# Kernel optimization log

Measured on AMD Instinct MI355X. Metric: run time of the kernel, lower is better.

## Reference

```python
import jax, jax.numpy as jnp
import numpy as np

NGRAM = 16
SUB = 512  # bytes per sub-block


def byte2image(block, ngram=NGRAM):
    """block: (B, L) int -> (B, 1, ngram*8, L-ngram) float32 in [-1, 1]."""
    B, L = block.shape
    blk = block.astype(jnp.int32)
    # nxt[:, i] = blk[:, i+1], last column zero
    nxt = jnp.concatenate([blk[:, 1:], jnp.zeros((B, 1), jnp.int32)], axis=1)
    # 8 bit-shifted views of the byte stream
    shifts = jnp.stack(
        [((blk << s) & 255) + ((nxt >> (8 - s)) & 255) for s in range(8)],
        axis=1,
    )  # (B, 8, L)
    flat = shifts.reshape(B, -1)  # (B, 8*L)
    parts = [flat] + [jnp.roll(flat, -i, axis=1) for i in range(1, ngram)]
    stacked = jnp.concatenate(parts, axis=1).reshape(B, ngram * 8, L)
    result = stacked[:, :, :-ngram].astype(jnp.float32)
    result = (result / 255.0 - 0.5) / 0.5
    return result[:, None]  # (B, 1, ngram*8, L-ngram)


def byte2image_4k(block, ngram=NGRAM):
    """block: (B, 4096) -> (B, 8, ngram*8, 512-ngram)."""
    return jnp.concatenate(
        [byte2image(block[:, i * SUB:(i + 1) * SUB], ngram) for i in range(8)],
        axis=1,
    )


def setup_inputs() -> dict:
    key = jax.random.key(0)
    kx, kw = jax.random.split(key)
    x = jax.random.randint(kx, (256, 4096), 0, 256, dtype=jnp.int64)
    W = jax.random.normal(kw, (496, 64), dtype=jnp.float32) * 0.02
    return {"x": x, "W": W}


def reference(x, W):
    # ByteFormerWrapper.forward with block_size=4096: byte2image_4k then the
    # (opaque) model; model stood in by a linear head over the image width.
    img = byte2image_4k(x)                      # (B, 8, 128, 496)
    out = jnp.einsum('bchw,wo->bcho', img, W)   # (B, 8, 128, 64)
    return out
```

## Files before the change

kernel.cpp:

```cpp
#include <hip/hip_runtime.h>

typedef unsigned short u16;
typedef unsigned int u32;
typedef _Float16 half8 __attribute__((ext_vector_type(8)));
typedef __attribute__((ext_vector_type(4))) float floatx4;

#define LSTRIDE 72
#define BIMG (128 * LSTRIDE)

__device__ __forceinline__ void gl_lds16(const void* g, void* l) {
  __builtin_amdgcn_global_load_lds(
      (const __attribute__((address_space(1))) void*)g,
      (__attribute__((address_space(3))) void*)l, 16, 0, 0);
}
__device__ __forceinline__ void gl_lds4(const void* g, void* l) {
  __builtin_amdgcn_global_load_lds(
      (const __attribute__((address_space(1))) void*)g,
      (__attribute__((address_space(3))) void*)l, 4, 0, 0);
}

__global__ __launch_bounds__(256) void byteformer_precompute(
    const float* __restrict__ Wm, u16* __restrict__ Bws,
    float* __restrict__ csumWs) {
  const int t = threadIdx.x;
  const int y = blockIdx.x >> 3, kc = blockIdx.x & 7;
  const int wave = t >> 6, o = t & 63;
  const int pp = wave >> 1, hf = wave & 1;
  u16* img = Bws + (size_t)blockIdx.x * BIMG;
  #pragma unroll
  for (int i = 0; i < 18; ++i) {
    const int kk = (hf * 18 + i) * 2;
    u32 val = 0u;
    if (kk < 64) {
      const int c0 = kc * 64 + kk - 2 * y - pp;
      const int c1 = c0 + 1;
      float f0 = (c0 >= 0 && c0 < 496) ? Wm[c0 * 64 + o] : 0.0f;
      float f1 = (c1 >= 0 && c1 < 496) ? Wm[c1 * 64 + o] : 0.0f;
      u16 h0 = __builtin_bit_cast(unsigned short, (_Float16)f0);
      u16 h1 = __builtin_bit_cast(unsigned short, (_Float16)f1);
      val = (u32)h0 | ((u32)h1 << 16);
    }
    *(u32*)&img[(pp * 64 + o) * LSTRIDE + kk] = val;
  }
  if (blockIdx.x == 0) {
    __shared__ float red[256];
    float s = 0.0f;
    for (int c = wave * 124; c < wave * 124 + 124; ++c) s += Wm[c * 64 + o];
    red[t] = s;
    __syncthreads();
    if (t < 64)
      csumWs[t] = (1024.0f * (2.0f / 255.0f) + 1.0f) *
                  (red[t] + red[t + 64] + red[t + 128] + red[t + 192]);
  }
}

__global__ __launch_bounds__(256, 4) void byteformer_fused(
    const int* __restrict__ x, const u16* __restrict__ Bws,
    const float* __restrict__ csumWs, float* __restrict__ out) {
  __shared__ __align__(16) u16 As[128 * LSTRIDE];
  __shared__ __align__(16) u16 Bs[128 * LSTRIDE];

  const int t = threadIdx.x;
  const int mtile = blockIdx.x;
  const int n0 = blockIdx.y * 128;

  const int wave = t >> 6, lane = t & 63;
  const int wm = wave >> 1, wn = wave & 1;
  const int quad = lane >> 4, l16 = lane & 15;

  const int sA_sub = t >> 4;
  const int sA_kg  = (t >> 1) & 7;
  const int sA_qh  = t & 1;
  const long xrow = ((long)mtile * 16 + sA_sub) * 512;

  const char* bimg0 = (const char*)(Bws + (size_t)blockIdx.y * 8 * BIMG);

  floatx4 acc[4][4];
  #pragma unroll
  for (int mt = 0; mt < 4; ++mt)
    #pragma unroll
    for (int nt = 0; nt < 4; ++nt)
      acc[mt][nt] = floatx4{0.f, 0.f, 0.f, 0.f};

  int4 ca, cb; int cc;
  {
    const int base = sA_kg * 8;
    ca = *(const int4*)&x[xrow + base];
    cb = *(const int4*)&x[xrow + base + 4];
    cc = x[xrow + base + 8];
  }

  for (int kc = 0; kc < 8; ++kc) {
    __syncthreads();

    {
      const char* src = bimg0 + (size_t)kc * (BIMG * 2);
      char* dst = (char*)Bs;
      const int woff = wave * 1024;
      #pragma unroll
      for (int j = 0; j < 4; ++j)
        gl_lds16(src + j * 4096 + woff + lane * 16, dst + j * 4096 + woff);
      const int woff4 = 16384 + wave * 256;
      #pragma unroll
      for (int j = 0; j < 2; ++j)
        gl_lds4(src + woff4 + j * 1024 + lane * 4, dst + woff4 + j * 1024);
    }

    {
      const u32 c0 = (u32)ca.x, c1 = (u32)ca.y, c2 = (u32)ca.z, c3 = (u32)ca.w;
      const u32 c4 = (u32)cb.x, c5 = (u32)cb.y, c6 = (u32)cb.z, c7 = (u32)cb.w;
      const u32 c8 = (u32)cc;
      const u32 P0 = ((c0 << 8) | c1) | (((c1 << 8) | c2) << 16);
      const u32 P1 = ((c2 << 8) | c3) | (((c3 << 8) | c4) << 16);
      const u32 P2 = ((c4 << 8) | c5) | (((c5 << 8) | c6) << 16);
      const u32 P3 = ((c6 << 8) | c7) | (((c7 << 8) | c8) << 16);
      u16* arow = &As[(sA_sub * 8 + sA_qh * 4) * LSTRIDE + sA_kg * 8];
      #pragma unroll
      for (int qi = 0; qi < 4; ++qi) {
        const int sh = 8 - (sA_qh * 4 + qi);
        int4 d;
        d.x = (int)(((P0 >> sh) & 0x00FF00FFu) | 0x64006400u);
        d.y = (int)(((P1 >> sh) & 0x00FF00FFu) | 0x64006400u);
        d.z = (int)(((P2 >> sh) & 0x00FF00FFu) | 0x64006400u);
        d.w = (int)(((P3 >> sh) & 0x00FF00FFu) | 0x64006400u);
        *(int4*)(arow + qi * LSTRIDE) = d;
      }
    }

    __syncthreads();

    if (kc < 7) {
      const int base = (kc + 1) * 64 + sA_kg * 8;
      ca = *(const int4*)&x[xrow + base];
      cb = *(const int4*)&x[xrow + base + 4];
      cc = (base + 8 < 512) ? x[xrow + base + 8] : 0;
    }

    #pragma unroll
    for (int ks = 0; ks < 2; ++ks) {
      const int koff = ks * 32 + quad * 8;
      half8 af[4], bf[4];
      #pragma unroll
      for (int mt = 0; mt < 4; ++mt)
        af[mt] = *(const half8*)&As[(wm * 64 + mt * 16 + l16) * LSTRIDE + koff];
      #pragma unroll
      for (int nt = 0; nt < 4; ++nt)
        bf[nt] = *(const half8*)&Bs[(wn * 64 + nt * 16 + l16) * LSTRIDE + koff];
      #pragma unroll
      for (int mt = 0; mt < 4; ++mt)
        #pragma unroll
        for (int nt = 0; nt < 4; ++nt)
          acc[mt][nt] = __builtin_amdgcn_mfma_f32_16x16x32_f16(
              af[mt], bf[nt], acc[mt][nt], 0, 0, 0);
    }
  }

  const float S = 2.0f / 255.0f;
  #pragma unroll
  for (int nt = 0; nt < 4; ++nt) {
    int n = n0 + wn * 64 + nt * 16 + l16;
    int p = n >> 6, o = n & 63;
    float cs = csumWs[o];
    #pragma unroll
    for (int mt = 0; mt < 4; ++mt) {
      int mbase = mtile * 128 + wm * 64 + mt * 16 + quad * 4;
      #pragma unroll
      for (int i = 0; i < 4; ++i) {
        int mr = mbase + i;
        int sub = mr >> 3, q = mr & 7;
        out[(long)sub * 8192 + (p * 8 + q) * 64 + o] = S * acc[mt][nt][i] - cs;
      }
    }
  }
}

extern "C" void kernel_launch(void* const* d_in, const int* in_sizes, int n_in,
                              void* d_out, int out_size, void* d_ws, size_t ws_size,
                              hipStream_t stream) {
  const int* x = (const int*)d_in[0];
  const float* Wm = (const float*)d_in[1];
  float* out = (float*)d_out;
  u16* Bws = (u16*)d_ws;
  float* csumWs = (float*)((char*)d_ws + (size_t)64 * BIMG * 2);
  byteformer_precompute<<<dim3(64), dim3(256), 0, stream>>>(Wm, Bws, csumWs);
  byteformer_fused<<<dim3(128, 8), dim3(256), 0, stream>>>(x, Bws, csumWs, out);
}
```

Baseline: 117.6 us.

## Double-buffer A/B LDS tiles and stage epilogue through LDS for coalesced stores

Allocates two LDS buffers each for the A and B tiles so that the next chunk's x load, B DMA and A bit-unpacking overlap with the current MFMA compute, cutting one barrier per iteration. The epilogue writes results into LDS and then issues coalesced float4 global stores instead of scattered scalar stores, with the csum values hoisted into registers. Launch bounds drop to 2 blocks per CU because LDS use doubles, which reduces occupancy in exchange for overlap.

```diff
diff --git a/kernel.cpp b/kernel.cpp
--- a/kernel.cpp
+++ b/kernel.cpp
@@ -54,15 +54,14 @@
   }
 }
 
-__global__ __launch_bounds__(256, 4) void byteformer_fused(
+__global__ __launch_bounds__(256, 2) void byteformer_fused(
     const int* __restrict__ x, const u16* __restrict__ Bws,
     const float* __restrict__ csumWs, float* __restrict__ out) {
-  __shared__ __align__(16) u16 As[128 * LSTRIDE];
-  __shared__ __align__(16) u16 Bs[128 * LSTRIDE];
+  __shared__ __align__(16) u16 arena[4 * BIMG];
 
   const int t = threadIdx.x;
   const int mtile = blockIdx.x;
-  const int n0 = blockIdx.y * 128;
+  const int y = blockIdx.y;
 
   const int wave = t >> 6, lane = t & 63;
   const int wm = wave >> 1, wn = wave & 1;
@@ -72,8 +71,7 @@
   const int sA_kg  = (t >> 1) & 7;
   const int sA_qh  = t & 1;
   const long xrow = ((long)mtile * 16 + sA_sub) * 512;
-
-  const char* bimg0 = (const char*)(Bws + (size_t)blockIdx.y * 8 * BIMG);
+  const char* bimg0 = (const char*)(Bws + (size_t)y * 8 * BIMG);
 
   floatx4 acc[4][4];
   #pragma unroll
@@ -82,70 +80,63 @@
     for (int nt = 0; nt < 4; ++nt)
       acc[mt][nt] = floatx4{0.f, 0.f, 0.f, 0.f};
 
+  float cs[4];
+  #pragma unroll
+  for (int nt = 0; nt < 4; ++nt) cs[nt] = csumWs[nt * 16 + l16];
+
   int4 ca, cb; int cc;
-  {
-    const int base = sA_kg * 8;
+  auto xload = [&](int kc) {
+    const int base = kc * 64 + sA_kg * 8;
     ca = *(const int4*)&x[xrow + base];
     cb = *(const int4*)&x[xrow + base + 4];
-    cc = x[xrow + base + 8];
-  }
-
-  for (int kc = 0; kc < 8; ++kc) {
-    __syncthreads();
-
-    {
-      const char* src = bimg0 + (size_t)kc * (BIMG * 2);
-      char* dst = (char*)Bs;
-      const int woff = wave * 1024;
-      #pragma unroll
-      for (int j = 0; j < 4; ++j)
-        gl_lds16(src + j * 4096 + woff + lane * 16, dst + j * 4096 + woff);
-      const int woff4 = 16384 + wave * 256;
-      #pragma unroll
-      for (int j = 0; j < 2; ++j)
-        gl_lds4(src + woff4 + j * 1024 + lane * 4, dst + woff4 + j * 1024);
-    }
-
-    {
-      const u32 c0 = (u32)ca.x, c1 = (u32)ca.y, c2 = (u32)ca.z, c3 = (u32)ca.w;
-      const u32 c4 = (u32)cb.x, c5 = (u32)cb.y, c6 = (u32)cb.z, c7 = (u32)cb.w;
-      const u32 c8 = (u32)cc;
-      const u32 P0 = ((c0 << 8) | c1) | (((c1 << 8) | c2) << 16);
-      const u32 P1 = ((c2 << 8) | c3) | (((c3 << 8) | c4) << 16);
-      const u32 P2 = ((c4 << 8) | c5) | (((c5 << 8) | c6) << 16);
-      const u32 P3 = ((c6 << 8) | c7) | (((c7 << 8) | c8) << 16);
-      u16* arow = &As[(sA_sub * 8 + sA_qh * 4) * LSTRIDE + sA_kg * 8];
-      #pragma unroll
-      for (int qi = 0; qi < 4; ++qi) {
-        const int sh = 8 - (sA_qh * 4 + qi);
-        int4 d;
-        d.x = (int)(((P0 >> sh) & 0x00FF00FFu) | 0x64006400u);
-        d.y = (int)(((P1 >> sh) & 0x00FF00FFu) | 0x64006400u);
-        d.z = (int)(((P2 >> sh) & 0x00FF00FFu) | 0x64006400u);
-        d.w = (int)(((P3 >> sh) & 0x00FF00FFu) | 0x64006400u);
-        *(int4*)(arow + qi * LSTRIDE) = d;
-      }
-    }
-
-    __syncthreads();
-
-    if (kc < 7) {
-      const int base = (kc + 1) * 64 + sA_kg * 8;
-      ca = *(const int4*)&x[xrow + base];
-      cb = *(const int4*)&x[xrow + base + 4];
-      cc = (base + 8 < 512) ? x[xrow + base + 8] : 0;
-    }
-
+    cc = (base + 8 < 512) ? x[xrow + base + 8] : 0;
+  };
+
+  auto bdma = [&](int kc, u16* dstb) {
+    const char* src = bimg0 + (size_t)kc * 18432;
+    char* dst = (char*)dstb;
+    const int woff = wave * 1024;
+    #pragma unroll
+    for (int j = 0; j < 4; ++j)
+      gl_lds16(src + j * 4096 + woff + lane * 16, dst + j * 4096 + woff);
+    const int woff4 = 16384 + wave * 256;
+    #pragma unroll
+    for (int j = 0; j < 2; ++j)
+      gl_lds4(src + woff4 + j * 1024 + lane * 4, dst + woff4 + j * 1024);
+  };
+
+  auto astage = [&](u16* dstb) {
+    const u32 c0 = (u32)ca.x, c1 = (u32)ca.y, c2 = (u32)ca.z, c3 = (u32)ca.w;
+    const u32 c4 = (u32)cb.x, c5 = (u32)cb.y, c6 = (u32)cb.z, c7 = (u32)cb.w;
+    const u32 c8 = (u32)cc;
+    const u32 P0 = ((c0 << 8) | c1) | (((c1 << 8) | c2) << 16);
+    const u32 P1 = ((c2 << 8) | c3) | (((c3 << 8) | c4) << 16);
+    const u32 P2 = ((c4 << 8) | c5) | (((c5 << 8) | c6) << 16);
+    const u32 P3 = ((c6 << 8) | c7) | (((c7 << 8) | c8) << 16);
+    u16* arow = &dstb[(sA_sub * 8 + sA_qh * 4) * LSTRIDE + sA_kg * 8];
+    #pragma unroll
+    for (int qi = 0; qi < 4; ++qi) {
+      const int sh = 8 - (sA_qh * 4 + qi);
+      int4 d;
+      d.x = (int)(((P0 >> sh) & 0x00FF00FFu) | 0x64006400u);
+      d.y = (int)(((P1 >> sh) & 0x00FF00FFu) | 0x64006400u);
+      d.z = (int)(((P2 >> sh) & 0x00FF00FFu) | 0x64006400u);
+      d.w = (int)(((P3 >> sh) & 0x00FF00FFu) | 0x64006400u);
+      *(int4*)(arow + qi * LSTRIDE) = d;
+    }
+  };
+
+  auto compute = [&](const u16* Ab, const u16* Bb) {
     #pragma unroll
     for (int ks = 0; ks < 2; ++ks) {
       const int koff = ks * 32 + quad * 8;
       half8 af[4], bf[4];
       #pragma unroll
       for (int mt = 0; mt < 4; ++mt)
-        af[mt] = *(const half8*)&As[(wm * 64 + mt * 16 + l16) * LSTRIDE + koff];
+        af[mt] = *(const half8*)&Ab[(wm * 64 + mt * 16 + l16) * LSTRIDE + koff];
       #pragma unroll
       for (int nt = 0; nt < 4; ++nt)
-        bf[nt] = *(const half8*)&Bs[(wn * 64 + nt * 16 + l16) * LSTRIDE + koff];
+        bf[nt] = *(const half8*)&Bb[(wn * 64 + nt * 16 + l16) * LSTRIDE + koff];
       #pragma unroll
       for (int mt = 0; mt < 4; ++mt)
         #pragma unroll
@@ -153,24 +144,50 @@
           acc[mt][nt] = __builtin_amdgcn_mfma_f32_16x16x32_f16(
               af[mt], bf[nt], acc[mt][nt], 0, 0, 0);
     }
-  }
-
+  };
+
+  bdma(0, arena + 2 * BIMG);
+  xload(0);
+  astage(arena);
+  __syncthreads();
+
+  #pragma unroll
+  for (int kc = 0; kc < 8; ++kc) {
+    u16* Acur = arena + (kc & 1) * BIMG;
+    u16* Bcur = arena + (2 + (kc & 1)) * BIMG;
+    u16* Anxt = arena + ((kc + 1) & 1) * BIMG;
+    u16* Bnxt = arena + (2 + ((kc + 1) & 1)) * BIMG;
+    if (kc < 7) {
+      xload(kc + 1);
+      bdma(kc + 1, Bnxt);
+    }
+    compute(Acur, Bcur);
+    if (kc < 7) astage(Anxt);
+    __syncthreads();
+  }
+
+  float* ep = (float*)arena;
   const float S = 2.0f / 255.0f;
   #pragma unroll
-  for (int nt = 0; nt < 4; ++nt) {
-    int n = n0 + wn * 64 + nt * 16 + l16;
-    int p = n >> 6, o = n & 63;
-    float cs = csumWs[o];
-    #pragma unroll
-    for (int mt = 0; mt < 4; ++mt) {
-      int mbase = mtile * 128 + wm * 64 + mt * 16 + quad * 4;
-      #pragma unroll
-      for (int i = 0; i < 4; ++i) {
-        int mr = mbase + i;
-        int sub = mr >> 3, q = mr & 7;
-        out[(long)sub * 8192 + (p * 8 + q) * 64 + o] = S * acc[mt][nt][i] - cs;
-      }
-    }
+  for (int mt = 0; mt < 4; ++mt) {
+    #pragma unroll
+    for (int i = 0; i < 4; ++i) {
+      const int mr = wm * 64 + mt * 16 + quad * 4 + i;
+      const int sub_l = mr >> 3, q = mr & 7;
+      const int rowbase = sub_l * 1040 + wn * 512 + q * 64 + l16;
+      #pragma unroll
+      for (int nt = 0; nt < 4; ++nt)
+        ep[rowbase + nt * 16] = S * acc[mt][nt][i] - cs[nt];
+    }
+  }
+  __syncthreads();
+
+  const long outbase = (long)mtile * 16 * 8192 + (long)y * 1024;
+  #pragma unroll
+  for (int k2 = 0; k2 < 16; ++k2) {
+    const float4 v =
+        *(const float4*)((const char*)ep + k2 * 4160 + wave * 1024 + lane * 16);
+    *(float4*)&out[outbase + (long)k2 * 8192 + wave * 256 + lane * 4] = v;
   }
 }
 
```

Result: no change. 119.5 us (+1.6%).
